# Kernel tuning notes

Measured on AMD Instinct MI355X. Metric: run time of the kernel, lower is better.

The kernel has to match this reference:

```python
import jax, jax.numpy as jnp
import numpy as np

N_NODES = 20000
N_EDGES = 320000
N_GRAPHS = 512
N_FEAT = 29
DIMS = [N_FEAT, 1024, 512, 256, 512, 1024]
EPS = 1e-5


def setup_inputs() -> dict:
    key = jax.random.key(0)
    ks = jax.random.split(key, 32)
    inp = {}
    inp["x"] = jax.random.normal(ks[0], (N_NODES, N_FEAT), dtype=jnp.float32)
    inp["edge_index"] = jax.random.randint(ks[1], (2, N_EDGES), 0, N_NODES, dtype=jnp.int64)
    inp["batch"] = jnp.sort(jax.random.randint(ks[2], (N_NODES,), 0, N_GRAPHS, dtype=jnp.int64))
    # 5 GCNConv layers: weight [in, out] + bias, plus BN gamma/beta
    for i in range(5):
        din, dout = DIMS[i], DIMS[i + 1]
        inp[f"W{i+1}"] = jax.random.normal(ks[3 + i], (din, dout), dtype=jnp.float32) * (1.0 / np.sqrt(din))
        inp[f"b{i+1}"] = jnp.zeros((dout,), dtype=jnp.float32)
        inp[f"g{i+1}"] = jnp.ones((dout,), dtype=jnp.float32)
        inp[f"be{i+1}"] = jnp.zeros((dout,), dtype=jnp.float32)
    # attention gate Linear(1024, 1)
    inp["Wg"] = jax.random.normal(ks[10], (1024, 1), dtype=jnp.float32) * 0.03
    inp["bg"] = jnp.zeros((1,), dtype=jnp.float32)
    # MLP head
    inp["Wf2"] = jax.random.normal(ks[11], (1024, 128), dtype=jnp.float32) * 0.03
    inp["bf2"] = jnp.zeros((128,), dtype=jnp.float32)
    inp["Wf3"] = jax.random.normal(ks[12], (128, 16), dtype=jnp.float32) * 0.25
    inp["bf3"] = jnp.zeros((16,), dtype=jnp.float32)
    inp["Wf4"] = jax.random.normal(ks[13], (16, 1), dtype=jnp.float32) * 0.25
    inp["bf4"] = jnp.zeros((1,), dtype=jnp.float32)
    return inp


def _gcn_conv(x, row, col, W, b):
    # PyG GCNConv: linear transform, then D^{-1/2}(A+I)D^{-1/2} aggregation, then bias.
    n = x.shape[0]
    xw = x @ W  # [N, dout]
    deg = jax.ops.segment_sum(jnp.ones_like(col, dtype=xw.dtype), col, num_segments=n)
    dinv = jnp.where(deg > 0, jax.lax.rsqrt(deg), 0.0)
    norm = dinv[row] * dinv[col]  # [E+N]
    out = jax.ops.segment_sum(xw[row] * norm[:, None], col, num_segments=n)
    return out + b


def _bn_train(x, gamma, beta):
    m = jnp.mean(x, axis=0)
    v = jnp.var(x, axis=0)  # biased, matches torch training normalization
    return gamma * (x - m) * jax.lax.rsqrt(v + EPS) + beta


def _global_attention(x, batch, Wg, bg, n_graphs):
    gate = (x @ Wg + bg)[:, 0]  # [N]
    gmax = jax.ops.segment_max(gate, batch, num_segments=n_graphs)
    e = jnp.exp(gate - gmax[batch])
    s = jax.ops.segment_sum(e, batch, num_segments=n_graphs)
    alpha = e / s[batch]
    return jax.ops.segment_sum(alpha[:, None] * x, batch, num_segments=n_graphs)


def reference(x, edge_index, batch,
              W1, b1, g1, be1, W2, b2, g2, be2, W3, b3, g3, be3,
              W4, b4, g4, be4, W5, b5, g5, be5,
              Wg, bg, Wf2, bf2, Wf3, bf3, Wf4, bf4):
    n = x.shape[0]
    sl = jnp.arange(n, dtype=edge_index.dtype)
    row = jnp.concatenate([edge_index[0], sl])  # with self-loops
    col = jnp.concatenate([edge_index[1], sl])
    h = x
    params = [(W1, b1, g1, be1), (W2, b2, g2, be2), (W3, b3, g3, be3),
              (W4, b4, g4, be4), (W5, b5, g5, be5)]
    for (W, b, g, be) in params:
        h = jax.nn.relu(_gcn_conv(h, row, col, W, b))
        h = _bn_train(h, g, be)
    p = _global_attention(h, batch, Wg, bg, N_GRAPHS)  # [G, 1024]
    p = jax.nn.relu(p @ Wf2 + bf2)
    p = jax.nn.relu(p @ Wf3 + bf3)
    return p @ Wf4 + bf4  # [G, 1]
```

## Files before the change

kernel.cpp:

```cpp
#include <hip/hip_runtime.h>

#define EPS_BN 1e-5f

constexpr int NN   = 20000;
constexpr int NE   = 320000;
constexpr int NTOT = NE + NN;
constexpr int NG   = 512;
constexpr int MPAD = 20480;
constexpr int NBLK = 79;

typedef _Float16 half8  __attribute__((ext_vector_type(8)));
typedef _Float16 half2v __attribute__((ext_vector_type(2)));
typedef float floatx4   __attribute__((ext_vector_type(4)));

__global__ void k_deg(const int* __restrict__ col, int* __restrict__ deg,
                      const int* __restrict__ batch, int* __restrict__ gcnt) {
  int e = blockIdx.x * blockDim.x + threadIdx.x;
  if (e >= NTOT) return;
  int c = (e < NE) ? col[e] : (e - NE);
  atomicAdd(&deg[c], 1);
  if (e < NN) atomicAdd(&gcnt[batch[e]], 1);
}

__global__ __launch_bounds__(256) void k_pre1(const int* __restrict__ deg,
                                              float* __restrict__ dinvv,
                                              int* __restrict__ psum) {
  __shared__ int ws[4];
  int t = threadIdx.x, lane = t & 63, wv = t >> 6;
  int idx = blockIdx.x * 256 + t;
  int d = (idx < NN) ? deg[idx] : 0;
  if (idx < NN) dinvv[idx] = rsqrtf((float)d);
  int s = d;
  for (int o = 1; o < 64; o <<= 1) { int u = __shfl_up(s, o, 64); if (lane >= o) s += u; }
  if (lane == 63) ws[wv] = s;
  __syncthreads();
  if (t == 0) psum[blockIdx.x] = ws[0] + ws[1] + ws[2] + ws[3];
}

__global__ __launch_bounds__(256) void k_pre2(const int* __restrict__ psum,
                                              int* __restrict__ pbase,
                                              const int* __restrict__ gcnt,
                                              int* __restrict__ goff) {
  __shared__ int ws[8];
  int t = threadIdx.x, lane = t & 63, wv = t >> 6;
  int v = (t < NBLK) ? psum[t] : 0;
  int inc = v;
  for (int o = 1; o < 64; o <<= 1) { int u = __shfl_up(inc, o, 64); if (lane >= o) inc += u; }
  if (lane == 63) ws[wv] = inc;
  __syncthreads();
  int base = 0;
  for (int w = 0; w < wv; ++w) base += ws[w];
  int excl = base + inc - v;
  if (t < NBLK) pbase[t] = excl;
  if (t == NBLK - 1) pbase[NBLK] = excl + v;
  __syncthreads();
  int a0 = gcnt[2 * t], a1 = gcnt[2 * t + 1];
  int p = a0 + a1;
  int incp = p;
  for (int o = 1; o < 64; o <<= 1) { int u = __shfl_up(incp, o, 64); if (lane >= o) incp += u; }
  if (lane == 63) ws[4 + wv] = incp;
  __syncthreads();
  int gb = 0;
  for (int w = 0; w < wv; ++w) gb += ws[4 + w];
  int exclp = gb + incp - p;
  goff[2 * t]     = exclp;
  goff[2 * t + 1] = exclp + a0;
  if (t == 255) goff[NG] = exclp + p;
}

__global__ __launch_bounds__(256) void k_pre3(const int* __restrict__ deg,
                                              const int* __restrict__ pbase,
                                              int* __restrict__ indptr,
                                              int* __restrict__ cursor) {
  __shared__ int ws[4];
  int t = threadIdx.x, lane = t & 63, wv = t >> 6;
  int idx = blockIdx.x * 256 + t;
  int d = (idx < NN) ? deg[idx] : 0;
  int inc = d;
  for (int o = 1; o < 64; o <<= 1) { int u = __shfl_up(inc, o, 64); if (lane >= o) inc += u; }
  if (lane == 63) ws[wv] = inc;
  __syncthreads();
  int base = pbase[blockIdx.x];
  for (int w = 0; w < wv; ++w) base += ws[w];
  int excl = base + inc - d;
  if (idx < NN) { indptr[idx] = excl; cursor[idx] = excl; }
  if (idx == NN - 1) indptr[NN] = excl + d;
}

__global__ void k_fill(const int* __restrict__ row, const int* __restrict__ col,
                       const float* __restrict__ dinv, int* __restrict__ cursor,
                       int2* __restrict__ csw, float* __restrict__ rsum) {
  int e = blockIdx.x * blockDim.x + threadIdx.x;
  if (e >= NTOT) return;
  int r, c;
  if (e < NE) { r = row[e]; c = col[e]; } else { r = c = e - NE; }
  float wv = dinv[r] * dinv[c];
  int pos = atomicAdd(&cursor[c], 1);
  int2 m; m.x = r; m.y = __builtin_bit_cast(int, wv);
  csw[pos] = m;
  atomicAdd(&rsum[c], wv);
}

__device__ __forceinline__ size_t fragoff(int n, int k, int kb) {
  return ((size_t)(n >> 4) * kb + (k >> 5)) * 512 + ((k >> 3) & 3) * 128 + (n & 15) * 8;
}

__global__ void k_wconv3(const float* __restrict__ W0, const float* __restrict__ W3,
                         const float* __restrict__ W4,
                         _Float16* __restrict__ T0, _Float16* __restrict__ T3,
                         _Float16* __restrict__ T4) {
  int c = blockIdx.x * blockDim.x + threadIdx.x;
  _Float16 ov[8];
  if (c < 4096) {
    int n = c >> 2, k = (c & 3) * 8;
    #pragma unroll
    for (int i = 0; i < 8; ++i)
      ov[i] = (_Float16)((k + i < 29) ? W0[(size_t)(k + i) * 1024 + n] : 0.f);
    *(uint4*)&T0[fragoff(n, k, 1)] = *(const uint4*)ov;
  } else if (c < 4096 + 16384) {
    int c2 = c - 4096;
    int n = c2 >> 5, k = (c2 & 31) * 8;
    #pragma unroll
    for (int i = 0; i < 8; ++i)
      ov[i] = (_Float16)W3[(size_t)(k + i) * 512 + n];
    *(uint4*)&T3[fragoff(n, k, 8)] = *(const uint4*)ov;
  } else if (c < 4096 + 16384 + 65536) {
    int c3 = c - 20480;
    int n = c3 >> 6, k = (c3 & 63) * 8;
    #pragma unroll
    for (int i = 0; i < 8; ++i)
      ov[i] = (_Float16)W4[(size_t)(k + i) * 1024 + n];
    *(uint4*)&T4[fragoff(n, k, 16)] = *(const uint4*)ov;
  }
}

__global__ __launch_bounds__(256) void k_wfold(const float* __restrict__ W, int K, int N,
                                               const float* __restrict__ sums,
                                               const float* __restrict__ gamma,
                                               const float* __restrict__ beta,
                                               _Float16* __restrict__ T,
                                               float* __restrict__ c) {
  __shared__ float red[256];
  int n = blockIdx.x, tid = threadIdx.x;
  int kb = K >> 5;
  const float inv_n = 1.f / NN;
  float csum = 0.f;
  for (int kc = tid; kc < (K >> 3); kc += 256) {
    int k = kc * 8;
    _Float16 ov[8];
    #pragma unroll
    for (int i = 0; i < 8; ++i) {
      int ki = k + i;
      float mean = sums[ki] * inv_n;
      float var  = sums[K + ki] * inv_n - mean * mean;
      float sc   = gamma[ki] * rsqrtf(var + EPS_BN);
      float sh   = beta[ki] - mean * sc;
      float wv   = W[(size_t)ki * N + n];
      ov[i] = (_Float16)(sc * wv);
      csum += sh * wv;
    }
    *(uint4*)&T[fragoff(n, k, kb)] = *(const uint4*)ov;
  }
  red[tid] = csum;
  __syncthreads();
  for (int o = 128; o > 0; o >>= 1) {
    if (tid < o) red[tid] += red[tid + o];
    __syncthreads();
  }
  if (tid == 0) c[n] = red[0];
}

#define AGG_CH 128
__global__ __launch_bounds__(128) void k_agg29(
    const float* __restrict__ X,
    const int* __restrict__ indptr, const int2* __restrict__ csw,
    _Float16* __restrict__ Y) {
  __shared__ int   s_src[AGG_CH];
  __shared__ float s_w[AGG_CH];
  __shared__ float red[128];
  int node = blockIdx.x;
  int tid  = threadIdx.x;
  int sub  = tid / 29;
  int feat = tid - sub * 29;
  bool act = tid < 116;
  int beg = indptr[node], end = indptr[node + 1];
  float acc = 0.f;
  for (int e0 = beg; e0 < end; e0 += AGG_CH) {
    int c = min(AGG_CH, end - e0);
    if (tid < c) {
      int2 m = csw[e0 + tid];
      s_src[tid] = m.x;
      s_w[tid]   = __builtin_bit_cast(float, m.y);
    }
    __syncthreads();
    if (act) {
      for (int j = 0; j < c; j += 4) {
        int jj = j + sub;
        if (jj < c) acc += s_w[jj] * X[(size_t)s_src[jj] * 29 + feat];
      }
    }
    __syncthreads();
  }
  red[tid] = acc;
  __syncthreads();
  if (tid < 32) {
    float v = 0.f;
    if (tid < 29) v = red[tid] + red[29 + tid] + red[58 + tid] + red[87 + tid];
    size_t fb = (size_t)(node >> 4) * 512 + (size_t)(tid >> 3) * 128 + (node & 15) * 8 + (tid & 7);
    Y[fb] = (_Float16)v;
  }
}

template<int MODE>
__global__ __launch_bounds__(256) void k_aggv(
    const _Float16* __restrict__ X,
    _Float16* __restrict__ Yf, _Float16* __restrict__ Yrow,
    const int* __restrict__ indptr, const int2* __restrict__ csw,
    const float* __restrict__ rowsum,
    const float* __restrict__ p0, const float* __restrict__ p1,
    const float* __restrict__ p2)
{
  constexpr int F = 512;
  int wave = threadIdx.x >> 6;
  int lane = threadIdx.x & 63;
  int node = blockIdx.x * 4 + wave;
  int beg = indptr[node], end = indptr[node + 1];
  float acc[8];
  #pragma unroll
  for (int i = 0; i < 8; ++i) acc[i] = 0.f;
  const unsigned* Xl = (const unsigned*)X + lane * 4;

  auto body = [&](int e) {
    int2 m = csw[e];
    float we = __builtin_bit_cast(float, m.y);
    uint4 d = *(const uint4*)(Xl + (size_t)m.x * (F / 2));
    unsigned uu[4] = {d.x, d.y, d.z, d.w};
    #pragma unroll
    for (int i = 0; i < 4; ++i) {
      half2v h = __builtin_bit_cast(half2v, uu[i]);
      acc[2 * i]     = fmaf(we, (float)h[0], acc[2 * i]);
      acc[2 * i + 1] = fmaf(we, (float)h[1], acc[2 * i + 1]);
    }
  };
  int e = beg;
  for (; e + 8 <= end; e += 8) {
    body(e); body(e + 1); body(e + 2); body(e + 3);
    body(e + 4); body(e + 5); body(e + 6); body(e + 7);
  }
  for (; e < end; ++e) body(e);

  float s_n = rowsum[node];
  _Float16 outv[8];
  #pragma unroll
  for (int i = 0; i < 8; ++i) {
    int f = lane * 8 + i;
    float v;
    if constexpr (MODE == 0) {
      v = fmaxf(acc[i] + s_n * p0[f] + p1[f], 0.f);
    } else {
      const float inv_n = 1.f / NN;
      float mean = p0[f] * inv_n;
      float var  = p0[F + f] * inv_n - mean * mean;
      float sc   = p1[f] * rsqrtf(var + EPS_BN);
      float sh   = p2[f] - mean * sc;
      v = sc * acc[i] + s_n * sh;
    }
    outv[i] = (_Float16)v;
  }
  if (Yf) {
    size_t fb = (size_t)(node >> 4) * (16 * 512) + lane * 128 + (node & 15) * 8;
    *(uint4*)(Yf + fb) = *(const uint4*)outv;
  }
  if (Yrow) {
    *(uint4*)(Yrow + (size_t)node * F + lane * 8) = *(const uint4*)outv;
  }
}

template<int MODE>
__global__ __launch_bounds__(256) void k_aggp(
    const _Float16* __restrict__ X,
    _Float16* __restrict__ Yf, _Float16* __restrict__ Yrow,
    const int* __restrict__ indptr, const int2* __restrict__ csw,
    const float* __restrict__ rowsum,
    const float* __restrict__ p0, const float* __restrict__ p1,
    const float* __restrict__ p2)
{
  constexpr int F = 256;
  int wave = threadIdx.x >> 6;
  int lane = threadIdx.x & 63;
  int half = lane >> 5;
  int l32  = lane & 31;
  int node = blockIdx.x * 8 + wave * 2 + half;
  int beg = indptr[node], end = indptr[node + 1];
  int len = end - beg;
  int len0 = __shfl(len, 0, 64);
  int len1 = __shfl(len, 32, 64);
  int maxlen = max(len0, len1);

  float acc[8];
  #pragma unroll
  for (int i = 0; i < 8; ++i) acc[i] = 0.f;
  const unsigned* Xl = (const unsigned*)X + l32 * 4;

  auto body = [&](int t) {
    int e = beg + min(t, len - 1);
    int2 m = csw[e];
    float we = (t < len) ? __builtin_bit_cast(float, m.y) : 0.f;
    uint4 d = *(const uint4*)(Xl + (size_t)m.x * (F / 2));
    unsigned uu[4] = {d.x, d.y, d.z, d.w};
    #pragma unroll
    for (int i = 0; i < 4; ++i) {
      half2v h = __builtin_bit_cast(half2v, uu[i]);
      acc[2 * i]     = fmaf(we, (float)h[0], acc[2 * i]);
      acc[2 * i + 1] = fmaf(we, (float)h[1], acc[2 * i + 1]);
    }
  };
  int t = 0;
  for (; t + 4 <= maxlen; t += 4) { body(t); body(t + 1); body(t + 2); body(t + 3); }
  for (; t < maxlen; ++t) body(t);

  float s_n = rowsum[node];
  _Float16 outv[8];
  #pragma unroll
  for (int i = 0; i < 8; ++i) {
    int f = l32 * 8 + i;
    float v;
    if constexpr (MODE == 0) {
      v = fmaxf(acc[i] + s_n * p0[f] + p1[f], 0.f);
    } else {
      const float inv_n = 1.f / NN;
      float mean = p0[f] * inv_n;
      float var  = p0[F + f] * inv_n - mean * mean;
      float sc   = p1[f] * rsqrtf(var + EPS_BN);
      float sh   = p2[f] - mean * sc;
      v = sc * acc[i] + s_n * sh;
    }
    outv[i] = (_Float16)v;
  }
  if (Yf) {
    size_t fb = (size_t)(node >> 4) * (8 * 512) + l32 * 128 + (node & 15) * 8;
    *(uint4*)(Yf + fb) = *(const uint4*)outv;
  }
  if (Yrow) {
    *(uint4*)(Yrow + (size_t)node * F + l32 * 8) = *(const uint4*)outv;
  }
}

template<int K, int FRAGOUT>
__global__ __launch_bounds__(256) void k_gemmf(
    const _Float16* __restrict__ Af, const _Float16* __restrict__ Bf,
    const float* __restrict__ bias,
    _Float16* __restrict__ Ch,
    _Float16* __restrict__ Cf,
    float* __restrict__ stats,
    int N, int do_relu, int nbx)
{
  __shared__ __align__(16) _Float16 cs[128 * 136];
  __shared__ float sred[256];

  const int tid  = threadIdx.x;
  const int wave = tid >> 6;
  const int lane = tid & 63;

  int lin = blockIdx.x;
  int xcd = lin & 7, seq = lin >> 3;
  int bx = seq % nbx, grp = seq / nbx;
  int by = xcd + 8 * grp;
  const int row0 = by * 128;
  const int col0 = bx * 128;

  const int q  = lane >> 4;
  const int mm = lane & 15;
  const int wm = wave >> 1;
  const int wn = wave & 1;

  sred[tid] = 0.f;

  constexpr int KB = K / 32;
  const _Float16* pa[4];
  const _Float16* pb[4];
  #pragma unroll
  for (int i = 0; i < 4; ++i)
    pa[i] = Af + (size_t)((row0 >> 4) + wm * 4 + i) * (KB * 512) + lane * 8;
  #pragma unroll
  for (int j = 0; j < 4; ++j)
    pb[j] = Bf + (size_t)((col0 >> 4) + wn * 4 + j) * (KB * 512) + lane * 8;

  floatx4 acc[4][4];
  #pragma unroll
  for (int i = 0; i < 4; ++i)
    #pragma unroll
    for (int j = 0; j < 4; ++j) acc[i][j] = floatx4{0.f, 0.f, 0.f, 0.f};

  half8 av[4], bv[4];
  #pragma unroll
  for (int i = 0; i < 4; ++i) { av[i] = *(const half8*)pa[i]; pa[i] += 512; }
  #pragma unroll
  for (int j = 0; j < 4; ++j) { bv[j] = *(const half8*)pb[j]; pb[j] += 512; }

  #pragma unroll 2
  for (int s = 0; s < KB; ++s) {
    half8 nav[4], nbv[4];
    if (s + 1 < KB) {
      #pragma unroll
      for (int i = 0; i < 4; ++i) { nav[i] = *(const half8*)pa[i]; pa[i] += 512; }
      #pragma unroll
      for (int j = 0; j < 4; ++j) { nbv[j] = *(const half8*)pb[j]; pb[j] += 512; }
    }
    #pragma unroll
    for (int j = 0; j < 4; ++j)
      #pragma unroll
      for (int i = 0; i < 4; ++i)
        acc[i][j] = __builtin_amdgcn_mfma_f32_16x16x32_f16(av[i], bv[j], acc[i][j], 0, 0, 0);
    if (s + 1 < KB) {
      #pragma unroll
      for (int i = 0; i < 4; ++i) av[i] = nav[i];
      #pragma unroll
      for (int j = 0; j < 4; ++j) bv[j] = nbv[j];
    }
  }

  __syncthreads();

  float sloc[4]  = {0.f, 0.f, 0.f, 0.f};
  float s2loc[4] = {0.f, 0.f, 0.f, 0.f};
  #pragma unroll
  for (int j = 0; j < 4; ++j) {
    int cl = wn * 64 + j * 16 + mm;
    float bvv = bias ? bias[col0 + cl] : 0.f;
    #pragma unroll
    for (int i = 0; i < 4; ++i) {
      #pragma unroll
      for (int r = 0; r < 4; ++r) {
        int rl = wm * 64 + i * 16 + q * 4 + r;
        float v = acc[i][j][r] + bvv;
        if (do_relu) v = fmaxf(v, 0.f);
        cs[rl * 136 + cl] = (_Float16)v;
        if (row0 + rl < NN) { sloc[j] += v; s2loc[j] += v * v; }
      }
    }
  }

  if (stats) {
    #pragma unroll
    for (int j = 0; j < 4; ++j) {
      float a = sloc[j], b2 = s2loc[j];
      a  += __shfl_xor(a, 16, 64);  a  += __shfl_xor(a, 32, 64);
      b2 += __shfl_xor(b2, 16, 64); b2 += __shfl_xor(b2, 32, 64);
      if (q == 0) {
        int cl = wn * 64 + j * 16 + mm;
        atomicAdd(&sred[cl], a);
        atomicAdd(&sred[128 + cl], b2);
      }
    }
  }
  __syncthreads();

  if (FRAGOUT) {
    int mlo = tid & 15, sub = (tid >> 4) & 3, kcr = (tid >> 6) & 3;
    int kbN = N >> 5;
    #pragma unroll
    for (int pass = 0; pass < 8; ++pass) {
      int m = pass * 16 + mlo;
      int kl = kcr * 32 + sub * 8;
      uint4 d = *(const uint4*)&cs[m * 136 + kl];
      size_t fa = ((size_t)((row0 >> 4) + pass) * kbN + (col0 >> 5) + kcr) * 512
                + sub * 128 + mlo * 8;
      *(uint4*)&Cf[fa] = d;
    }
  } else {
    #pragma unroll
    for (int pass = 0; pass < 8; ++pass) {
      int cidx = tid + pass * 256;
      int r = cidx >> 4, kc = cidx & 15;
      int rr = row0 + r;
      if (rr < NN) {
        uint4 d = *(const uint4*)&cs[r * 136 + kc * 8];
        *(uint4*)&Ch[(size_t)rr * N + col0 + kc * 8] = d;
      }
    }
  }

  if (stats && tid < 128) {
    atomicAdd(&stats[col0 + tid], sred[tid]);
    atomicAdd(&stats[N + col0 + tid], sred[128 + tid]);
  }
}

template<int F>
__global__ __launch_bounds__(256) void k_statsf(const _Float16* __restrict__ Xf,
                                                float* __restrict__ sums) {
  constexpr int KB = F / 32;
  constexpr int NT = NN / 16;
  int wid  = (blockIdx.x * 256 + threadIdx.x) >> 6;
  int lane = threadIdx.x & 63;
  int nw   = (gridDim.x * 256) >> 6;
  int kidx = wid % KB;
  int ng0  = wid / KB;
  int step = nw / KB;
  int sub = lane >> 4, n16 = lane & 15;

  float s[8], s2[8];
  #pragma unroll
  for (int i = 0; i < 8; ++i) { s[i] = 0.f; s2[i] = 0.f; }

  for (int ng = ng0; ng < NT; ng += step) {
    const _Float16* p = Xf + ((size_t)ng * KB + kidx) * 512 + lane * 8;
    uint4 d = *(const uint4*)p;
    unsigned uu[4] = {d.x, d.y, d.z, d.w};
    #pragma unroll
    for (int i = 0; i < 4; ++i) {
      half2v h = __builtin_bit_cast(half2v, uu[i]);
      float v0 = (float)h[0], v1 = (float)h[1];
      s[2 * i]      += v0;  s2[2 * i]     += v0 * v0;
      s[2 * i + 1]  += v1;  s2[2 * i + 1] += v1 * v1;
    }
  }
  #pragma unroll
  for (int o = 1; o < 16; o <<= 1) {
    #pragma unroll
    for (int i = 0; i < 8; ++i) {
      s[i]  += __shfl_xor(s[i],  o, 64);
      s2[i] += __shfl_xor(s2[i], o, 64);
    }
  }
  if (n16 == 0) {
    int f = kidx * 32 + sub * 8;
    #pragma unroll
    for (int i = 0; i < 8; ++i) {
      atomicAdd(&sums[f + i], s[i]);
      atomicAdd(&sums[F + f + i], s2[i]);
    }
  }
}

__global__ __launch_bounds__(256) void k_stats16(const _Float16* __restrict__ X, int F,
                                                 float* __restrict__ sums) {
  int tid = threadIdx.x;
  int npf = F >> 8;
  float s[2] = {0.f, 0.f}, s2[2] = {0.f, 0.f};
  for (int r = blockIdx.x; r < NN; r += gridDim.x) {
    #pragma unroll
    for (int i = 0; i < 2; ++i) {
      if (i < npf) {
        float v = (float)X[(size_t)r * F + tid + i * 256];
        s[i] += v; s2[i] += v * v;
      }
    }
  }
  #pragma unroll
  for (int i = 0; i < 2; ++i) {
    if (i < npf) {
      atomicAdd(&sums[tid + i * 256], s[i]);
      atomicAdd(&sums[F + tid + i * 256], s2[i]);
    }
  }
}

__global__ __launch_bounds__(256) void k_gate2(const _Float16* __restrict__ X,
                                               const float* __restrict__ sums,
                                               const float* __restrict__ g5,
                                               const float* __restrict__ be5,
                                               const float* __restrict__ Wg,
                                               const float* __restrict__ bg,
                                               float* __restrict__ gate) {
  __shared__ float red[512];
  int n = blockIdx.x, tid = threadIdx.x;
  int f = tid * 4;
  const float inv_n = 1.f / NN;
  uint2 u = *(const uint2*)(X + (size_t)n * 1024 + f);
  half2v h0 = __builtin_bit_cast(half2v, u.x);
  half2v h1 = __builtin_bit_cast(half2v, u.y);
  float xv[4] = {(float)h0[0], (float)h0[1], (float)h1[0], (float)h1[1]};
  float s = 0.f, t = 0.f;
  #pragma unroll
  for (int i = 0; i < 4; ++i) {
    int ff = f + i;
    float mean = sums[ff] * inv_n;
    float var  = sums[1024 + ff] * inv_n - mean * mean;
    float sc   = g5[ff] * rsqrtf(var + EPS_BN);
    float sh   = be5[ff] - mean * sc;
    float wg   = Wg[ff];
    s += xv[i] * (sc * wg);
    t += sh * wg;
  }
  red[tid] = s;
  red[256 + tid] = t;
  __syncthreads();
  for (int o = 128; o > 0; o >>= 1) {
    if (tid < o) { red[tid] += red[tid + o]; red[256 + tid] += red[256 + tid + o]; }
    __syncthreads();
  }
  if (tid == 0) gate[n] = red[0] + red[256] + bg[0];
}

__global__ __launch_bounds__(256) void k_poolhead(
    const _Float16* __restrict__ X, const float* __restrict__ gate,
    const int* __restrict__ goff,
    const float* __restrict__ sums, const float* __restrict__ g5,
    const float* __restrict__ be5,
    const float* __restrict__ Wf2, const float* __restrict__ bf2,
    const float* __restrict__ Wf3, const float* __restrict__ bf3,
    const float* __restrict__ Wf4, const float* __restrict__ bf4,
    float* __restrict__ out)
{
  __shared__ float red[256];
  __shared__ float sp[1024];
  __shared__ float sp2[128];
  __shared__ float sp3[16];
  int g = blockIdx.x, tid = threadIdx.x;
  int beg = goff[g], end = goff[g + 1];
  bool nonempty = end > beg;

  float m = -3.4e38f;
  for (int n = beg + tid; n < end; n += 256) m = fmaxf(m, gate[n]);
  red[tid] = m;
  __syncthreads();
  for (int o = 128; o > 0; o >>= 1) {
    if (tid < o) red[tid] = fmaxf(red[tid], red[tid + o]);
    __syncthreads();
  }
  m = red[0];
  __syncthreads();
  float s = 0.f;
  for (int n = beg + tid; n < end; n += 256) s += expf(gate[n] - m);
  red[tid] = s;
  __syncthreads();
  for (int o = 128; o > 0; o >>= 1) {
    if (tid < o) red[tid] += red[tid + o];
    __syncthreads();
  }
  float inv = nonempty ? (1.f / red[0]) : 0.f;

  int f = tid * 4;
  const float inv_n = 1.f / NN;
  float acc[4] = {0.f, 0.f, 0.f, 0.f};
  if (nonempty) {
    const _Float16* Xf = X + f;
    int n = beg;
    for (; n + 4 <= end; n += 4) {
      float a0 = expf(gate[n]     - m);
      float a1 = expf(gate[n + 1] - m);
      float a2 = expf(gate[n + 2] - m);
      float a3 = expf(gate[n + 3] - m);
      uint2 u0 = *(const uint2*)(Xf + (size_t)(n)     * 1024);
      uint2 u1 = *(const uint2*)(Xf + (size_t)(n + 1) * 1024);
      uint2 u2 = *(const uint2*)(Xf + (size_t)(n + 2) * 1024);
      uint2 u3 = *(const uint2*)(Xf + (size_t)(n + 3) * 1024);
      half2v p00 = __builtin_bit_cast(half2v, u0.x), p01 = __builtin_bit_cast(half2v, u0.y);
      half2v p10 = __builtin_bit_cast(half2v, u1.x), p11 = __builtin_bit_cast(half2v, u1.y);
      half2v p20 = __builtin_bit_cast(half2v, u2.x), p21 = __builtin_bit_cast(half2v, u2.y);
      half2v p30 = __builtin_bit_cast(half2v, u3.x), p31 = __builtin_bit_cast(half2v, u3.y);
      acc[0] += a0 * (float)p00[0] + a1 * (float)p10[0] + a2 * (float)p20[0] + a3 * (float)p30[0];
      acc[1] += a0 * (float)p00[1] + a1 * (float)p10[1] + a2 * (float)p20[1] + a3 * (float)p30[1];
      acc[2] += a0 * (float)p01[0] + a1 * (float)p11[0] + a2 * (float)p21[0] + a3 * (float)p31[0];
      acc[3] += a0 * (float)p01[1] + a1 * (float)p11[1] + a2 * (float)p21[1] + a3 * (float)p31[1];
    }
    for (; n < end; ++n) {
      float a = expf(gate[n] - m);
      uint2 u0 = *(const uint2*)(Xf + (size_t)n * 1024);
      half2v p0 = __builtin_bit_cast(half2v, u0.x), p1 = __builtin_bit_cast(half2v, u0.y);
      acc[0] += a * (float)p0[0];
      acc[1] += a * (float)p0[1];
      acc[2] += a * (float)p1[0];
      acc[3] += a * (float)p1[1];
    }
  }
  #pragma unroll
  for (int i = 0; i < 4; ++i) {
    int ff = f + i;
    float mean = sums[ff] * inv_n;
    float var  = sums[1024 + ff] * inv_n - mean * mean;
    float sc   = g5[ff] * rsqrtf(var + EPS_BN);
    float sh   = be5[ff] - mean * sc;
    sp[ff] = nonempty ? (acc[i] * inv * sc + sh) : 0.f;
  }
  __syncthreads();

  if (tid < 128) {
    float s2 = bf2[tid];
    for (int k = 0; k < 1024; ++k) s2 += sp[k] * Wf2[k * 128 + tid];
    sp2[tid] = fmaxf(s2, 0.f);
  }
  __syncthreads();
  if (tid < 16) {
    float t = bf3[tid];
    for (int k = 0; k < 128; ++k) t += sp2[k] * Wf3[k * 16 + tid];
    sp3[tid] = fmaxf(t, 0.f);
  }
  __syncthreads();
  if (tid == 0) {
    float t = bf4[0];
    for (int k = 0; k < 16; ++k) t += sp3[k] * Wf4[k];
    out[g] = t;
  }
}

extern "C" void kernel_launch(void* const* d_in, const int* in_sizes, int n_in,
                              void* d_out, int out_size, void* d_ws, size_t ws_size,
                              hipStream_t stream) {
  const float* x     = (const float*)d_in[0];
  const int*   ei    = (const int*)d_in[1];
  const int*   batch = (const int*)d_in[2];
  const float* W[5]; const float* b[5]; const float* g[5]; const float* be[5];
  for (int l = 0; l < 5; ++l) {
    W[l]  = (const float*)d_in[3 + 4 * l];
    b[l]  = (const float*)d_in[4 + 4 * l];
    g[l]  = (const float*)d_in[5 + 4 * l];
    be[l] = (const float*)d_in[6 + 4 * l];
  }
  const float* Wg  = (const float*)d_in[23];
  const float* bg  = (const float*)d_in[24];
  const float* Wf2 = (const float*)d_in[25];
  const float* bf2 = (const float*)d_in[26];
  const float* Wf3 = (const float*)d_in[27];
  const float* bf3 = (const float*)d_in[28];
  const float* Wf4 = (const float*)d_in[29];
  const float* bf4 = (const float*)d_in[30];
  float* out = (float*)d_out;

  const int* row = ei;
  const int* col = ei + NE;

  char* base = (char*)d_ws;
  size_t off = 0;
  auto alloc = [&](size_t bytes) -> char* {
    char* p = base + off;
    off = (off + bytes + 255) & ~(size_t)255;
    return p;
  };
  _Float16*  AH  = (_Float16*)alloc((size_t)MPAD * 1024 * 2);
  _Float16*  AF  = (_Float16*)alloc((size_t)MPAD * 512 * 2);
  _Float16*  ASM = (_Float16*)alloc((size_t)MPAD * 32 * 2);
  _Float16*  BF  = (_Float16*)alloc((size_t)NN * 512 * 2);
  _Float16*  BF2 = (_Float16*)alloc((size_t)NN * 512 * 2);
  _Float16*  H5  = (_Float16*)alloc((size_t)NN * 1024 * 2);
  const int wtsz[5] = {1024 * 32, 512 * 1024, 256 * 512, 512 * 256, 1024 * 512};
  _Float16* WT[5];
  for (int l = 0; l < 5; ++l) WT[l] = (_Float16*)alloc((size_t)wtsz[l] * 2);
  float* c2  = (float*)alloc(512 * 4);
  float* c3  = (float*)alloc(256 * 4);
  float* dinv    = (float*)alloc(NN * 4);
  int*   indptr  = (int*)alloc((NN + 1) * 4);
  int*   cursor  = (int*)alloc(NN * 4);
  int2*  csw     = (int2*)alloc((size_t)NTOT * 8);
  int*   psum    = (int*)alloc((NBLK + 1) * 4);
  int*   pbase   = (int*)alloc((NBLK + 1) * 4);
  int*   goff    = (int*)alloc((NG + 1) * 4);
  float* gate    = (float*)alloc(NN * 4);
  size_t znf = 6656 + NN + NG + NN;
  float* zbase = (float*)alloc(znf * 4);
  float* bns  = zbase;
  int*   deg  = (int*)(zbase + 6656);
  int*   gcnt = (int*)(zbase + 6656 + NN);
  float* rsum = zbase + 6656 + NN + NG;
  float* bns1 = bns;
  float* bns2 = bns + 2048;
  float* bns3 = bns + 3072;
  float* bns4 = bns + 3584;
  float* bns5 = bns + 4608;

  hipMemsetAsync(zbase, 0, znf * 4, stream);
  k_deg<<<(NTOT + 255) / 256, 256, 0, stream>>>(col, deg, batch, gcnt);
  k_pre1<<<NBLK, 256, 0, stream>>>(deg, dinv, psum);
  k_pre2<<<1, 256, 0, stream>>>(psum, pbase, gcnt, goff);
  k_pre3<<<NBLK, 256, 0, stream>>>(deg, pbase, indptr, cursor);
  k_fill<<<(NTOT + 255) / 256, 256, 0, stream>>>(row, col, dinv, cursor, csw, rsum);
  k_wconv3<<<336, 256, 0, stream>>>(W[0], W[3], W[4], WT[0], WT[3], WT[4]);

  k_agg29<<<NN, 128, 0, stream>>>(x, indptr, csw, ASM);
  k_gemmf<32, 1><<<8 * 160, 256, 0, stream>>>(ASM, WT[0], b[0], nullptr, AH, bns1, 1024, 1, 8);

  k_wfold<<<512, 256, 0, stream>>>(W[1], 1024, 512, bns1, g[0], be[0], WT[1], c2);
  k_gemmf<1024, 0><<<4 * 160, 256, 0, stream>>>(AH, WT[1], nullptr, BF, nullptr, nullptr, 512, 0, 4);
  k_aggv<0><<<NN / 4, 256, 0, stream>>>(BF, AF, nullptr, indptr, csw, rsum, c2, b[1], nullptr);
  k_statsf<512><<<256, 256, 0, stream>>>(AF, bns2);

  k_wfold<<<256, 256, 0, stream>>>(W[2], 512, 256, bns2, g[1], be[1], WT[2], c3);
  k_gemmf<512, 0><<<2 * 160, 256, 0, stream>>>(AF, WT[2], nullptr, BF2, nullptr, nullptr, 256, 0, 2);
  k_aggp<0><<<NN / 8, 256, 0, stream>>>(BF2, nullptr, BF, indptr, csw, rsum, c3, b[2], nullptr);
  k_stats16<<<512, 256, 0, stream>>>(BF, 256, bns3);

  k_aggp<1><<<NN / 8, 256, 0, stream>>>(BF, AH, nullptr, indptr, csw, rsum, bns3, g[2], be[2]);
  k_gemmf<256, 0><<<4 * 160, 256, 0, stream>>>(AH, WT[3], b[3], BF2, nullptr, bns4, 512, 1, 4);

  k_aggv<1><<<NN / 4, 256, 0, stream>>>(BF2, AF, nullptr, indptr, csw, rsum, bns4, g[3], be[3]);
  k_gemmf<512, 0><<<8 * 160, 256, 0, stream>>>(AF, WT[4], b[4], H5, nullptr, bns5, 1024, 1, 8);

  k_gate2<<<NN, 256, 0, stream>>>(H5, bns5, g[4], be[4], Wg, bg, gate);
  k_poolhead<<<NG, 256, 0, stream>>>(H5, gate, goff, bns5, g[4], be[4],
                                     Wf2, bf2, Wf3, bf3, Wf4, bf4, out);
}
```

Baseline: 587.5 us.

## Replace per-node vector aggregation with feature-chunked scalar gather kernel

Merges the 512- and 256-wide aggregation kernels into one templated kernel. Each block now covers a 64-feature chunk for 16 nodes, and each lane gathers a single fp16 element per edge, where before a wave handled a whole node row with 16-byte vector loads. Fragment-layout output goes through a shared-memory tile for the transpose. The aim is to improve cache locality per feature chunk and cut divergence, but it issues many more narrow 2-byte gather loads and re-reads the CSR entries once per chunk.

```diff
diff --git a/kernel.cpp b/kernel.cpp
--- a/kernel.cpp
+++ b/kernel.cpp
@@ -211,138 +211,79 @@
   }
 }
 
-template<int MODE>
-__global__ __launch_bounds__(256) void k_aggv(
-    const _Float16* __restrict__ X,
-    _Float16* __restrict__ Yf, _Float16* __restrict__ Yrow,
+template<int F, int MODE, int ROWOUT>
+__global__ __launch_bounds__(256) void k_aggc(
+    const _Float16* __restrict__ X, _Float16* __restrict__ Y,
     const int* __restrict__ indptr, const int2* __restrict__ csw,
     const float* __restrict__ rowsum,
     const float* __restrict__ p0, const float* __restrict__ p1,
     const float* __restrict__ p2)
 {
-  constexpr int F = 512;
-  int wave = threadIdx.x >> 6;
-  int lane = threadIdx.x & 63;
-  int node = blockIdx.x * 4 + wave;
-  int beg = indptr[node], end = indptr[node + 1];
-  float acc[8];
-  #pragma unroll
-  for (int i = 0; i < 8; ++i) acc[i] = 0.f;
-  const unsigned* Xl = (const unsigned*)X + lane * 4;
-
-  auto body = [&](int e) {
-    int2 m = csw[e];
-    float we = __builtin_bit_cast(float, m.y);
-    uint4 d = *(const uint4*)(Xl + (size_t)m.x * (F / 2));
-    unsigned uu[4] = {d.x, d.y, d.z, d.w};
-    #pragma unroll
-    for (int i = 0; i < 4; ++i) {
-      half2v h = __builtin_bit_cast(half2v, uu[i]);
-      acc[2 * i]     = fmaf(we, (float)h[0], acc[2 * i]);
-      acc[2 * i + 1] = fmaf(we, (float)h[1], acc[2 * i + 1]);
-    }
-  };
-  int e = beg;
-  for (; e + 8 <= end; e += 8) {
-    body(e); body(e + 1); body(e + 2); body(e + 3);
-    body(e + 4); body(e + 5); body(e + 6); body(e + 7);
-  }
-  for (; e < end; ++e) body(e);
-
-  float s_n = rowsum[node];
-  _Float16 outv[8];
-  #pragma unroll
-  for (int i = 0; i < 8; ++i) {
-    int f = lane * 8 + i;
+  constexpr int NCH = F / 64;
+  constexpr int KB  = F / 32;
+  __shared__ _Float16 sm[16][72];
+  int lin   = blockIdx.x;
+  int chunk = lin & (NCH - 1);
+  int ng    = lin / NCH;
+  int wave  = threadIdx.x >> 6;
+  int lane  = threadIdx.x & 63;
+  int fbase = chunk * 64;
+  int f     = fbase + lane;
+  const _Float16* Xc = X + fbase + lane;
+  const float inv_n = 1.f / NN;
+
+  float sc = 0.f, sh = 0.f, c0 = 0.f, c1 = 0.f;
+  if constexpr (MODE == 0) {
+    c0 = p0[f]; c1 = p1[f];
+  } else {
+    float mean = p0[f] * inv_n;
+    float var  = p0[F + f] * inv_n - mean * mean;
+    sc = p1[f] * rsqrtf(var + EPS_BN);
+    sh = p2[f] - mean * sc;
+  }
+
+  #pragma unroll
+  for (int ni = 0; ni < 4; ++ni) {
+    int node = ng * 16 + wave * 4 + ni;
+    int beg = indptr[node], end = indptr[node + 1];
+    float a0 = 0.f, a1 = 0.f;
+    int e = beg;
+    for (; e + 8 <= end; e += 8) {
+      #pragma unroll
+      for (int u = 0; u < 8; u += 2) {
+        int2 m0 = csw[e + u];
+        int2 m1 = csw[e + u + 1];
+        a0 = fmaf(__builtin_bit_cast(float, m0.y), (float)Xc[(size_t)m0.x * F], a0);
+        a1 = fmaf(__builtin_bit_cast(float, m1.y), (float)Xc[(size_t)m1.x * F], a1);
+      }
+    }
+    for (; e < end; ++e) {
+      int2 m = csw[e];
+      a0 = fmaf(__builtin_bit_cast(float, m.y), (float)Xc[(size_t)m.x * F], a0);
+    }
+    float acc = a0 + a1;
+    float s_n = rowsum[node];
     float v;
-    if constexpr (MODE == 0) {
-      v = fmaxf(acc[i] + s_n * p0[f] + p1[f], 0.f);
+    if constexpr (MODE == 0) v = fmaxf(acc + s_n * c0 + c1, 0.f);
+    else                     v = sc * acc + s_n * sh;
+    if constexpr (ROWOUT) {
+      Y[(size_t)node * F + f] = (_Float16)v;
     } else {
-      const float inv_n = 1.f / NN;
-      float mean = p0[f] * inv_n;
-      float var  = p0[F + f] * inv_n - mean * mean;
-      float sc   = p1[f] * rsqrtf(var + EPS_BN);
-      float sh   = p2[f] - mean * sc;
-      v = sc * acc[i] + s_n * sh;
-    }
-    outv[i] = (_Float16)v;
-  }
-  if (Yf) {
-    size_t fb = (size_t)(node >> 4) * (16 * 512) + lane * 128 + (node & 15) * 8;
-    *(uint4*)(Yf + fb) = *(const uint4*)outv;
-  }
-  if (Yrow) {
-    *(uint4*)(Yrow + (size_t)node * F + lane * 8) = *(const uint4*)outv;
-  }
-}
-
-template<int MODE>
-__global__ __launch_bounds__(256) void k_aggp(
-    const _Float16* __restrict__ X,
-    _Float16* __restrict__ Yf, _Float16* __restrict__ Yrow,
-    const int* __restrict__ indptr, const int2* __restrict__ csw,
-    const float* __restrict__ rowsum,
-    const float* __restrict__ p0, const float* __restrict__ p1,
-    const float* __restrict__ p2)
-{
-  constexpr int F = 256;
-  int wave = threadIdx.x >> 6;
-  int lane = threadIdx.x & 63;
-  int half = lane >> 5;
-  int l32  = lane & 31;
-  int node = blockIdx.x * 8 + wave * 2 + half;
-  int beg = indptr[node], end = indptr[node + 1];
-  int len = end - beg;
-  int len0 = __shfl(len, 0, 64);
-  int len1 = __shfl(len, 32, 64);
-  int maxlen = max(len0, len1);
-
-  float acc[8];
-  #pragma unroll
-  for (int i = 0; i < 8; ++i) acc[i] = 0.f;
-  const unsigned* Xl = (const unsigned*)X + l32 * 4;
-
-  auto body = [&](int t) {
-    int e = beg + min(t, len - 1);
-    int2 m = csw[e];
-    float we = (t < len) ? __builtin_bit_cast(float, m.y) : 0.f;
-    uint4 d = *(const uint4*)(Xl + (size_t)m.x * (F / 2));
-    unsigned uu[4] = {d.x, d.y, d.z, d.w};
-    #pragma unroll
-    for (int i = 0; i < 4; ++i) {
-      half2v h = __builtin_bit_cast(half2v, uu[i]);
-      acc[2 * i]     = fmaf(we, (float)h[0], acc[2 * i]);
-      acc[2 * i + 1] = fmaf(we, (float)h[1], acc[2 * i + 1]);
-    }
-  };
-  int t = 0;
-  for (; t + 4 <= maxlen; t += 4) { body(t); body(t + 1); body(t + 2); body(t + 3); }
-  for (; t < maxlen; ++t) body(t);
-
-  float s_n = rowsum[node];
-  _Float16 outv[8];
-  #pragma unroll
-  for (int i = 0; i < 8; ++i) {
-    int f = l32 * 8 + i;
-    float v;
-    if constexpr (MODE == 0) {
-      v = fmaxf(acc[i] + s_n * p0[f] + p1[f], 0.f);
-    } else {
-      const float inv_n = 1.f / NN;
-      float mean = p0[f] * inv_n;
-      float var  = p0[F + f] * inv_n - mean * mean;
-      float sc   = p1[f] * rsqrtf(var + EPS_BN);
-      float sh   = p2[f] - mean * sc;
-      v = sc * acc[i] + s_n * sh;
-    }
-    outv[i] = (_Float16)v;
-  }
-  if (Yf) {
-    size_t fb = (size_t)(node >> 4) * (8 * 512) + l32 * 128 + (node & 15) * 8;
-    *(uint4*)(Yf + fb) = *(const uint4*)outv;
-  }
-  if (Yrow) {
-    *(uint4*)(Yrow + (size_t)node * F + l32 * 8) = *(const uint4*)outv;
+      sm[wave * 4 + ni][lane] = (_Float16)v;
+    }
+  }
+
+  if constexpr (!ROWOUT) {
+    __syncthreads();
+    int tid = threadIdx.x;
+    if (tid < 128) {
+      int tile = tid >> 6, n16 = tid & 15, sub = (tid >> 4) & 3;
+      _Float16 ov[8];
+      #pragma unroll
+      for (int i = 0; i < 8; ++i) ov[i] = sm[n16][tile * 32 + sub * 8 + i];
+      size_t fa = ((size_t)ng * KB + chunk * 2 + tile) * 512 + sub * 128 + n16 * 8;
+      *(uint4*)&Y[fa] = *(const uint4*)ov;
+    }
   }
 }
 
@@ -773,18 +714,18 @@
 
   k_wfold<<<512, 256, 0, stream>>>(W[1], 1024, 512, bns1, g[0], be[0], WT[1], c2);
   k_gemmf<1024, 0><<<4 * 160, 256, 0, stream>>>(AH, WT[1], nullptr, BF, nullptr, nullptr, 512, 0, 4);
-  k_aggv<0><<<NN / 4, 256, 0, stream>>>(BF, AF, nullptr, indptr, csw, rsum, c2, b[1], nullptr);
+  k_aggc<512, 0, 0><<<1250 * 8, 256, 0, stream>>>(BF, AF, indptr, csw, rsum, c2, b[1], nullptr);
   k_statsf<512><<<256, 256, 0, stream>>>(AF, bns2);
 
   k_wfold<<<256, 256, 0, stream>>>(W[2], 512, 256, bns2, g[1], be[1], WT[2], c3);
   k_gemmf<512, 0><<<2 * 160, 256, 0, stream>>>(AF, WT[2], nullptr, BF2, nullptr, nullptr, 256, 0, 2);
-  k_aggp<0><<<NN / 8, 256, 0, stream>>>(BF2, nullptr, BF, indptr, csw, rsum, c3, b[2], nullptr);
+  k_aggc<256, 0, 1><<<1250 * 4, 256, 0, stream>>>(BF2, BF, indptr, csw, rsum, c3, b[2], nullptr);
   k_stats16<<<512, 256, 0, stream>>>(BF, 256, bns3);
 
-  k_aggp<1><<<NN / 8, 256, 0, stream>>>(BF, AH, nullptr, indptr, csw, rsum, bns3, g[2], be[2]);
+  k_aggc<256, 1, 0><<<1250 * 4, 256, 0, stream>>>(BF, AH, indptr, csw, rsum, bns3, g[2], be[2]);
   k_gemmf<256, 0><<<4 * 160, 256, 0, stream>>>(AH, WT[3], b[3], BF2, nullptr, bns4, 512, 1, 4);
 
-  k_aggv<1><<<NN / 4, 256, 0, stream>>>(BF2, AF, nullptr, indptr, csw, rsum, bns4, g[3], be[3]);
+  k_aggc<512, 1, 0><<<1250 * 8, 256, 0, stream>>>(BF2, AF, indptr, csw, rsum, bns4, g[3], be[3]);
   k_gemmf<512, 0><<<8 * 160, 256, 0, stream>>>(AF, WT[4], b[4], H5, nullptr, bns5, 1024, 1, 8);
 
   k_gate2<<<NN, 256, 0, stream>>>(H5, bns5, g[4], be[4], Wg, bg, gate);
```

Result: slower. 709.1 us (+20.7%).
